# Kernel tuning notes

Measured on AMD Instinct MI355X. Metric: run time of the kernel, lower is better.

The kernel has to match this reference:

```python
import jax, jax.numpy as jnp
from jax import lax
import numpy as np
import math

D_STATE = 2
D_CONV = 4

def _ln(x, g, b, eps=1e-5):
    m = x.mean(-1, keepdims=True)
    v = ((x - m) ** 2).mean(-1, keepdims=True)
    return (x - m) * lax.rsqrt(v + eps) * g + b

def _mamba(x, Win, convw, convb, Wx, Wdt, bdt, Alog, Dp, Wout):
    # x: (b, L, d_model); expand=1 so d_inner == d_model
    b, L, dm = x.shape
    di = Win.shape[0] // 2
    n = Alog.shape[1]
    dtr = Wdt.shape[1]
    k = convw.shape[-1]
    xz = x @ Win.T                                   # (b, L, 2*di)
    xi, z = xz[..., :di], xz[..., di:]
    # causal depthwise conv1d along the sequence axis (pad left k-1, truncate to L)
    xc = jnp.pad(xi, ((0, 0), (k - 1, 0), (0, 0))).transpose(0, 2, 1)  # (b, di, L+k-1)
    xc = lax.conv_general_dilated(xc, convw, (1,), 'VALID',
                                  dimension_numbers=('NCH', 'OIH', 'NCH'),
                                  feature_group_count=di)
    xi = jax.nn.silu(xc.transpose(0, 2, 1) + convb)  # (b, L, di)
    dbl = xi @ Wx.T                                  # (b, L, dtr + 2n)
    dt = jax.nn.softplus(dbl[..., :dtr] @ Wdt.T + bdt)   # (b, L, di)
    Bm = dbl[..., dtr:dtr + n]                       # (b, L, n)
    Cm = dbl[..., dtr + n:]                          # (b, L, n)
    A = -jnp.exp(Alog)                               # (di, n)
    dA = jnp.exp(dt[..., None] * A)                  # (b, L, di, n)
    dBx = dt[..., None] * Bm[:, :, None, :] * xi[..., None]  # (b, L, di, n)

    def step(h, inp):
        dA_t, dBx_t, C_t = inp
        h = dA_t * h + dBx_t                         # (b, di, n)
        return h, jnp.einsum('bdn,bn->bd', h, C_t)

    h0 = jnp.zeros((b, di, n), x.dtype)
    _, ys = lax.scan(step, h0, (dA.transpose(1, 0, 2, 3),
                                dBx.transpose(1, 0, 2, 3),
                                Cm.transpose(1, 0, 2)))
    y = ys.transpose(1, 0, 2) + Dp * xi              # (b, L, di)
    y = y * jax.nn.silu(z)
    return y @ Wout.T                                # (b, L, out_c)

def setup_inputs():
    key = jax.random.key(0)
    ks = jax.random.split(key, 32)
    B, C, H, W = 16, 256, 32, 32
    dm = H * W
    di = dm                      # expand = 1
    dtr = math.ceil(dm / 16)     # dt_rank = 64
    n, k = D_STATE, D_CONV

    def rn(i, shape, s):
        return (jax.random.normal(ks[i], shape) * s).astype(jnp.float32)

    inp = {'x': rn(0, (B, C, H, W), 1.0)}

    def mamba_p(pfx, base):
        inp[pfx + 'Win'] = rn(base, (2 * di, dm), dm ** -0.5)
        inp[pfx + 'convw'] = rn(base + 1, (di, 1, k), k ** -0.5)
        inp[pfx + 'convb'] = jnp.zeros((di,), jnp.float32)
        inp[pfx + 'Wx'] = rn(base + 2, (dtr + 2 * n, di), di ** -0.5)
        inp[pfx + 'Wdt'] = rn(base + 3, (di, dtr), dtr ** -0.5)
        inp[pfx + 'bdt'] = rn(base + 4, (di,), 0.1)
        inp[pfx + 'Alog'] = jnp.log(jnp.broadcast_to(
            jnp.arange(1, n + 1, dtype=jnp.float32), (di, n)))
        inp[pfx + 'D'] = jnp.ones((di,), jnp.float32)
        inp[pfx + 'Wout'] = rn(base + 5, (dm, di), di ** -0.5)  # out_c = sp_dim2^2 = dm

    mamba_p('m1_', 1)
    mamba_p('m2_', 8)
    inp['ln1_g'] = jnp.ones((dm,), jnp.float32)
    inp['ln1_b'] = jnp.zeros((dm,), jnp.float32)
    inp['ln2_g'] = jnp.ones((dm,), jnp.float32)
    inp['ln2_b'] = jnp.zeros((dm,), jnp.float32)
    inp['W_mid'] = rn(15, (C, C), C ** -0.5)   # Linear_Layer inside LIFM_SPA (bias=False)
    inp['W_spa'] = rn(16, (dm, dm), dm ** -0.5)  # linear_spa (nn.Linear default bias)
    inp['b_spa'] = jnp.zeros((dm,), jnp.float32)
    inp['W_res'] = rn(17, (C, C), C ** -0.5)   # lin_chan in residual path (bias=False)
    return inp

def reference(x, m1_Win, m1_convw, m1_convb, m1_Wx, m1_Wdt, m1_bdt, m1_Alog, m1_D, m1_Wout,
              m2_Win, m2_convw, m2_convb, m2_Wx, m2_Wdt, m2_bdt, m2_Alog, m2_D, m2_Wout,
              ln1_g, ln1_b, ln2_g, ln2_b, W_mid, W_spa, b_spa, W_res):
    b, c, h, w = x.shape
    hw = h * w
    # LIFM_SPA path: SSM_spa -> Linear_Layer (channel mix + SiLU) -> SSM_spa
    s = _mamba(x.reshape(b, c, hw), m1_Win, m1_convw, m1_convb,
               m1_Wx, m1_Wdt, m1_bdt, m1_Alog, m1_D, m1_Wout)
    s = _ln(s, ln1_g, ln1_b)                               # (b, c, hw)
    s = jax.nn.silu(jnp.einsum('bcs,oc->bos', s, W_mid))   # channel linear, SiLU (dropout off in eval)
    s = _mamba(s, m2_Win, m2_convw, m2_convb,
               m2_Wx, m2_Wdt, m2_bdt, m2_Alog, m2_D, m2_Wout)
    s = _ln(s, ln2_g, ln2_b)                               # (b, out_c, hw)
    # residual path: spatial linear (+bias) + SiLU, then channel linear + SiLU
    r = jax.nn.silu(x.reshape(b, c, hw) @ W_spa.T + b_spa)
    r = jax.nn.silu(jnp.einsum('bcs,oc->bos', r, W_res))
    return jax.nn.silu(s + r).reshape(b, -1, h, w)
```

## Files before the change

### kernel.cpp

```cpp
#include <hip/hip_runtime.h>
#include <math.h>

#define BATCH 16
#define LSEQ  256
#define DM    1024
#define DI    1024
#define NROWS (BATCH*LSEQ)
#define DTR   64
#define TWO_DI 2048
#define NCH   16
#define CHL   16

typedef __attribute__((ext_vector_type(8))) short short8;
typedef __attribute__((ext_vector_type(4))) float floatx4;
typedef __attribute__((ext_vector_type(4))) unsigned short ushortx4;

__device__ __forceinline__ float siluf(float x) {
    return x / (1.0f + __expf(-x));
}
__device__ __forceinline__ float softplusf(float x) {
    return fmaxf(x, 0.0f) + log1pf(__expf(-fabsf(x)));
}
__device__ __forceinline__ unsigned short f2bf(float f) {
    unsigned int u = __float_as_uint(f);
    u += 0x7fffu + ((u >> 16) & 1u);
    return (unsigned short)(u >> 16);
}
__device__ __forceinline__ float bf2f(unsigned short s) {
    return __uint_as_float(((unsigned int)s) << 16);
}
__device__ __forceinline__ void async16(const short* g, short* l) {
    __builtin_amdgcn_global_load_lds(
        (const __attribute__((address_space(1))) unsigned int*)g,
        (__attribute__((address_space(3))) unsigned int*)l,
        16, 0, 0);
}

__global__ __launch_bounds__(256) void cast8(
    const float* __restrict__ x,    unsigned short* __restrict__ ox,
    const float* __restrict__ w1i,  unsigned short* __restrict__ o1i,
    const float* __restrict__ w1o,  unsigned short* __restrict__ o1o,
    const float* __restrict__ w2i,  unsigned short* __restrict__ o2i,
    const float* __restrict__ w2o,  unsigned short* __restrict__ o2o,
    const float* __restrict__ wsp,  unsigned short* __restrict__ osp,
    const float* __restrict__ wmd,  unsigned short* __restrict__ omd,
    const float* __restrict__ wrs,  unsigned short* __restrict__ ors)
{
    const int b = blockIdx.x;
    const float* in; unsigned short* out; int base;
    if      (b <  4096) { in = x;   out = ox;  base = 0; }
    else if (b <  6144) { in = w1i; out = o1i; base = 4096; }
    else if (b <  7168) { in = w1o; out = o1o; base = 6144; }
    else if (b <  9216) { in = w2i; out = o2i; base = 7168; }
    else if (b < 10240) { in = w2o; out = o2o; base = 9216; }
    else if (b < 11264) { in = wsp; out = osp; base = 10240; }
    else if (b < 11328) { in = wmd; out = omd; base = 11264; }
    else                { in = wrs; out = ors; base = 11328; }
    const size_t i = ((size_t)(b - base) * 256 + threadIdx.x) * 4;
    const float4 v = *(const float4*)(in + i);
    union { unsigned short s[4]; unsigned long long u; } p;
    p.s[0] = f2bf(v.x); p.s[1] = f2bf(v.y);
    p.s[2] = f2bf(v.z); p.s[3] = f2bf(v.w);
    *(unsigned long long*)(out + i) = p.u;
}

template <int EP, int OUT16, int BATW, int FIN>
__global__ __launch_bounds__(64) void gemm1w(
    const short* __restrict__ A,
    const short* __restrict__ W,
    const float* __restrict__ bias,
    const float* __restrict__ Sadd,
    void* __restrict__ Cout,
    int M, int N, int K)
{
    __shared__ short As[2 * 64 * 32];
    __shared__ short Bs[2 * 64 * 32];

    const int bz = BATW ? blockIdx.z : 0;
    const short* Wb = W + (size_t)bz * N * K;
    const size_t cbase = (size_t)bz * M * N;

    const int lane = threadIdx.x;
    const int row0 = blockIdx.y * 64;
    const int col0 = blockIdx.x * 64;

    const int srow  = lane >> 2;
    const int skoff = (lane & 3) * 8;
    const short* gA = A  + (size_t)(row0 + srow) * K + skoff;
    const short* gB = Wb + (size_t)(col0 + srow) * K + skoff;
    short* lA = As + srow * 32 + skoff;
    short* lB = Bs + srow * 32 + skoff;

    const int fr = lane & 15;
    const int fk = (lane >> 4) * 8;

    floatx4 acc[4][4] = {};

    #pragma unroll
    for (int r = 0; r < 4; r++) {
        async16(gA + (size_t)(r * 16) * K, lA + r * 16 * 32);
        async16(gB + (size_t)(r * 16) * K, lB + r * 16 * 32);
    }
    __syncthreads();

    int cur = 0;
    for (int k0 = 0; k0 < K; k0 += 32) {
        const short* Ac = As + cur * 64 * 32;
        const short* Bc = Bs + cur * 64 * 32;
        short8 af[4], bfr[4];
        #pragma unroll
        for (int t = 0; t < 4; t++) {
            af[t]  = *(const short8*)&Ac[(t * 16 + fr) * 32 + fk];
            bfr[t] = *(const short8*)&Bc[(t * 16 + fr) * 32 + fk];
        }
        if (k0 + 32 < K) {
            const int nb = cur ^ 1;
            #pragma unroll
            for (int r = 0; r < 4; r++) {
                async16(gA + (size_t)(r * 16) * K + k0 + 32, lA + (nb * 64 + r * 16) * 32);
                async16(gB + (size_t)(r * 16) * K + k0 + 32, lB + (nb * 64 + r * 16) * 32);
            }
        }
        #pragma unroll
        for (int i = 0; i < 4; i++)
            #pragma unroll
            for (int j = 0; j < 4; j++)
                acc[i][j] = __builtin_amdgcn_mfma_f32_16x16x32_bf16(
                    af[i], bfr[j], acc[i][j], 0, 0, 0);
        __syncthreads();
        cur ^= 1;
    }

    const int crow = row0 + (lane >> 4) * 4;
    const int ccol = col0 + (lane & 15);
    #pragma unroll
    for (int i = 0; i < 4; i++) {
        #pragma unroll
        for (int j = 0; j < 4; j++) {
            const int c = ccol + j * 16;
            #pragma unroll
            for (int r = 0; r < 4; r++) {
                float v = acc[i][j][r];
                if (EP == 1) v = softplusf(v + bias[c]);
                else if (EP == 2) v = siluf(v + bias[c]);
                else if (EP == 3) v = siluf(v);
                const size_t idx = cbase + (size_t)(crow + i * 16 + r) * N + c;
                if (FIN) v = siluf(Sadd[idx] + v);
                if (OUT16) ((unsigned short*)Cout)[idx] = f2bf(v);
                else       ((float*)Cout)[idx] = v;
            }
        }
    }
}

__global__ __launch_bounds__(256) void gemm_nn_wcomb(
    const float* __restrict__ Wdt1, const float* __restrict__ Wx1,
    unsigned short* __restrict__ C1,
    const float* __restrict__ Wdt2, const float* __restrict__ Wx2,
    unsigned short* __restrict__ C2)
{
    const float* Wdt = blockIdx.z ? Wdt2 : Wdt1;
    const float* Wx  = blockIdx.z ? Wx2  : Wx1;
    unsigned short* C16 = blockIdx.z ? C2 : C1;

    __shared__ float Asf[16][64];
    __shared__ float Bsf[16][64];

    const int tid = threadIdx.x;
    const int tx = tid & 15;
    const int ty = tid >> 4;
    const int row0 = blockIdx.y * 64;
    const int col0 = blockIdx.x * 64;
    const int lrow = tid >> 2;
    const int lcol = (tid & 3) * 4;
    const int bk = tid >> 4;
    const int bn = (tid & 15) * 4;

    float acc[4][4] = {};

    for (int k0 = 0; k0 < 64; k0 += 16) {
        const float4 av = *(const float4*)(Wdt + (size_t)(row0 + lrow) * 64 + k0 + lcol);
        Asf[lcol + 0][lrow] = av.x;
        Asf[lcol + 1][lrow] = av.y;
        Asf[lcol + 2][lrow] = av.z;
        Asf[lcol + 3][lrow] = av.w;
        *(float4*)&Bsf[bk][bn] = *(const float4*)(Wx + (size_t)(k0 + bk) * 1024 + col0 + bn);
        __syncthreads();

        #pragma unroll
        for (int kk = 0; kk < 16; kk++) {
            const float4 a = *(const float4*)&Asf[kk][ty * 4];
            const float4 b = *(const float4*)&Bsf[kk][tx * 4];
            const float af[4] = {a.x, a.y, a.z, a.w};
            const float bfv[4] = {b.x, b.y, b.z, b.w};
            #pragma unroll
            for (int i = 0; i < 4; i++)
                #pragma unroll
                for (int j = 0; j < 4; j++)
                    acc[i][j] = fmaf(af[i], bfv[j], acc[i][j]);
        }
        __syncthreads();
    }

    #pragma unroll
    for (int i = 0; i < 4; i++) {
        const int r = row0 + ty * 4 + i;
        #pragma unroll
        for (int j = 0; j < 4; j++)
            C16[(size_t)r * 1024 + col0 + tx * 4 + j] = f2bf(acc[i][j]);
    }
}

__global__ __launch_bounds__(256) void conv_silu_bc(
    const unsigned short* __restrict__ xz16,
    const float* __restrict__ convw,
    const float* __restrict__ convb,
    const float* __restrict__ Wx,
    unsigned short* __restrict__ xi16,
    float* __restrict__ bc)
{
    __shared__ float redc[4][4];
    const int r = blockIdx.x;
    const int l = r & (LSEQ - 1);
    const int tid = threadIdx.x;
    const int d0 = tid * 4;

    ushortx4 x0 = *(const ushortx4*)(xz16 + (size_t)r * TWO_DI + d0);
    ushortx4 x1 = {0,0,0,0}, x2 = {0,0,0,0}, x3 = {0,0,0,0};
    if (l >= 1) x1 = *(const ushortx4*)(xz16 + (size_t)(r - 1) * TWO_DI + d0);
    if (l >= 2) x2 = *(const ushortx4*)(xz16 + (size_t)(r - 2) * TWO_DI + d0);
    if (l >= 3) x3 = *(const ushortx4*)(xz16 + (size_t)(r - 3) * TWO_DI + d0);

    float p0 = 0.f, p1 = 0.f, p2 = 0.f, p3 = 0.f;
    ushortx4 outv;
    #pragma unroll
    for (int j = 0; j < 4; j++) {
        const int d = d0 + j;
        const float4 w = *(const float4*)(convw + d * 4);
        float acc = w.w * bf2f(x0[j]);
        acc = fmaf(w.z, bf2f(x1[j]), acc);
        acc = fmaf(w.y, bf2f(x2[j]), acc);
        acc = fmaf(w.x, bf2f(x3[j]), acc);
        const float v = siluf(acc + convb[d]);
        outv[j] = f2bf(v);
        p0 = fmaf(v, Wx[64 * 1024 + d], p0);
        p1 = fmaf(v, Wx[65 * 1024 + d], p1);
        p2 = fmaf(v, Wx[66 * 1024 + d], p2);
        p3 = fmaf(v, Wx[67 * 1024 + d], p3);
    }
    *(ushortx4*)(xi16 + (size_t)r * DI + d0) = outv;

    #pragma unroll
    for (int o = 32; o; o >>= 1) {
        p0 += __shfl_down(p0, o, 64);
        p1 += __shfl_down(p1, o, 64);
        p2 += __shfl_down(p2, o, 64);
        p3 += __shfl_down(p3, o, 64);
    }
    const int w = tid >> 6, lane = tid & 63;
    if (lane == 0) {
        redc[w][0] = p0; redc[w][1] = p1; redc[w][2] = p2; redc[w][3] = p3;
    }
    __syncthreads();
    if (tid < 4)
        bc[r * 4 + tid] = redc[0][tid] + redc[1][tid] + redc[2][tid] + redc[3][tid];
}

__global__ __launch_bounds__(256) void scan_part1(
    const unsigned short* __restrict__ dt16,
    const unsigned short* __restrict__ xi16,
    const float* __restrict__ bc,
    const float* __restrict__ Alog,
    float4* __restrict__ hc)
{
    const int d  = blockIdx.x * 256 + threadIdx.x;
    const int b  = blockIdx.y;
    const int ch = blockIdx.z;
    const float A0 = -__expf(Alog[d * 2 + 0]);
    const float A1 = -__expf(Alog[d * 2 + 1]);
    float h0 = 0.f, h1 = 0.f, p0 = 1.f, p1 = 1.f;
    const int r0 = b * LSEQ + ch * CHL;
    #pragma unroll 4
    for (int l = 0; l < CHL; l++) {
        const int r = r0 + l;
        const float dtv = bf2f(dt16[(size_t)r * DI + d]);
        const float xiv = bf2f(xi16[(size_t)r * DI + d]);
        const float4 bcv = *(const float4*)(bc + r * 4);
        const float e0 = __expf(dtv * A0);
        const float e1 = __expf(dtv * A1);
        const float dbx = dtv * xiv;
        h0 = fmaf(e0, h0, dbx * bcv.x);
        h1 = fmaf(e1, h1, dbx * bcv.y);
        p0 *= e0; p1 *= e1;
    }
    hc[(size_t)(b * NCH + ch) * DI + d] = make_float4(h0, h1, p0, p1);
}

__global__ __launch_bounds__(256) void scan_carry(
    const float4* __restrict__ hc,
    float2* __restrict__ ci)
{
    const int d = blockIdx.x * 256 + threadIdx.x;
    const int b = blockIdx.y;
    float c0 = 0.f, c1 = 0.f;
    #pragma unroll
    for (int ch = 0; ch < NCH; ch++) {
        const size_t idx = (size_t)(b * NCH + ch) * DI + d;
        const float4 v = hc[idx];
        ci[idx] = make_float2(c0, c1);
        c0 = fmaf(v.z, c0, v.x);
        c1 = fmaf(v.w, c1, v.y);
    }
}

__global__ __launch_bounds__(256) void scan_part2(
    const unsigned short* __restrict__ dt16,
    const unsigned short* __restrict__ xi16,
    const unsigned short* __restrict__ xz16,
    const float* __restrict__ bc,
    const float* __restrict__ Alog,
    const float* __restrict__ Dp,
    const float2* __restrict__ ci,
    unsigned short* __restrict__ yg16)
{
    const int d  = blockIdx.x * 256 + threadIdx.x;
    const int b  = blockIdx.y;
    const int ch = blockIdx.z;
    const float A0 = -__expf(Alog[d * 2 + 0]);
    const float A1 = -__expf(Alog[d * 2 + 1]);
    const float Dv = Dp[d];
    const float2 c = ci[(size_t)(b * NCH + ch) * DI + d];
    float h0 = c.x, h1 = c.y;
    const int r0 = b * LSEQ + ch * CHL;
    #pragma unroll 4
    for (int l = 0; l < CHL; l++) {
        const int r = r0 + l;
        const float dtv = bf2f(dt16[(size_t)r * DI + d]);
        const float xiv = bf2f(xi16[(size_t)r * DI + d]);
        const float4 bcv = *(const float4*)(bc + r * 4);
        const float zv = bf2f(xz16[(size_t)r * TWO_DI + DI + d]);
        const float e0 = __expf(dtv * A0);
        const float e1 = __expf(dtv * A1);
        const float dbx = dtv * xiv;
        h0 = fmaf(e0, h0, dbx * bcv.x);
        h1 = fmaf(e1, h1, dbx * bcv.y);
        const float y = fmaf(h0, bcv.z, fmaf(h1, bcv.w, Dv * xiv));
        yg16[(size_t)r * DI + d] = f2bf(y * siluf(zv));
    }
}

__global__ __launch_bounds__(256) void ln_kernel(
    float* __restrict__ s,
    const float* __restrict__ g,
    const float* __restrict__ bb)
{
    __shared__ float red[8];
    const size_t base = (size_t)blockIdx.x * DM;
    const int t = threadIdx.x;
    float x0 = s[base + t];
    float x1 = s[base + t + 256];
    float x2 = s[base + t + 512];
    float x3 = s[base + t + 768];
    float sum = x0 + x1 + x2 + x3;
    #pragma unroll
    for (int o = 32; o; o >>= 1) sum += __shfl_down(sum, o, 64);
    const int w = t >> 6, lane = t & 63;
    if (lane == 0) red[w] = sum;
    __syncthreads();
    const float m = (red[0] + red[1] + red[2] + red[3]) * (1.0f / 1024.0f);
    const float d0 = x0 - m, d1 = x1 - m, d2 = x2 - m, d3 = x3 - m;
    float ss = d0 * d0 + d1 * d1 + d2 * d2 + d3 * d3;
    #pragma unroll
    for (int o = 32; o; o >>= 1) ss += __shfl_down(ss, o, 64);
    if (lane == 0) red[4 + w] = ss;
    __syncthreads();
    const float var = (red[4] + red[5] + red[6] + red[7]) * (1.0f / 1024.0f);
    const float inv = rsqrtf(var + 1e-5f);
    s[base + t]       = d0 * inv * g[t]       + bb[t];
    s[base + t + 256] = d1 * inv * g[t + 256] + bb[t + 256];
    s[base + t + 512] = d2 * inv * g[t + 512] + bb[t + 512];
    s[base + t + 768] = d3 * inv * g[t + 768] + bb[t + 768];
}

__global__ __launch_bounds__(256) void transpose_cast(
    const float* __restrict__ in, unsigned short* __restrict__ out)
{
    __shared__ float tile[32][33];
    const int b = blockIdx.z;
    const int c0 = blockIdx.y * 32;
    const int s0 = blockIdx.x * 32;
    const int tx = threadIdx.x & 31;
    const int ty = threadIdx.x >> 5;
    const size_t ib = (size_t)b * 256 * 1024;
    const size_t ob = (size_t)b * 1024 * 256;
    #pragma unroll
    for (int i = 0; i < 4; i++)
        tile[tx][ty + i * 8] = in[ib + (size_t)(c0 + ty + i * 8) * 1024 + s0 + tx];
    __syncthreads();
    #pragma unroll
    for (int i = 0; i < 4; i++)
        out[ob + (size_t)(s0 + ty + i * 8) * 256 + c0 + tx] = f2bf(tile[ty + i * 8][tx]);
}

__global__ __launch_bounds__(256) void transpose16(
    const unsigned short* __restrict__ in, unsigned short* __restrict__ out)
{
    __shared__ unsigned short tile[32][34];
    const int b = blockIdx.z;
    const int c0 = blockIdx.y * 32;
    const int s0 = blockIdx.x * 32;
    const int tx = threadIdx.x & 31;
    const int ty = threadIdx.x >> 5;
    const size_t ib = (size_t)b * 256 * 1024;
    const size_t ob = (size_t)b * 1024 * 256;
    #pragma unroll
    for (int i = 0; i < 4; i++)
        tile[tx][ty + i * 8] = in[ib + (size_t)(c0 + ty + i * 8) * 1024 + s0 + tx];
    __syncthreads();
    #pragma unroll
    for (int i = 0; i < 4; i++)
        out[ob + (size_t)(s0 + ty + i * 8) * 256 + c0 + tx] = tile[ty + i * 8][tx];
}

extern "C" void kernel_launch(void* const* d_in, const int* in_sizes, int n_in,
                              void* d_out, int out_size, void* d_ws, size_t ws_size,
                              hipStream_t stream)
{
    const float* x        = (const float*)d_in[0];
    const float* m1_Win   = (const float*)d_in[1];
    const float* m1_convw = (const float*)d_in[2];
    const float* m1_convb = (const float*)d_in[3];
    const float* m1_Wx    = (const float*)d_in[4];
    const float* m1_Wdt   = (const float*)d_in[5];
    const float* m1_bdt   = (const float*)d_in[6];
    const float* m1_Alog  = (const float*)d_in[7];
    const float* m1_D     = (const float*)d_in[8];
    const float* m1_Wout  = (const float*)d_in[9];
    const float* m2_Win   = (const float*)d_in[10];
    const float* m2_convw = (const float*)d_in[11];
    const float* m2_convb = (const float*)d_in[12];
    const float* m2_Wx    = (const float*)d_in[13];
    const float* m2_Wdt   = (const float*)d_in[14];
    const float* m2_bdt   = (const float*)d_in[15];
    const float* m2_Alog  = (const float*)d_in[16];
    const float* m2_D     = (const float*)d_in[17];
    const float* m2_Wout  = (const float*)d_in[18];
    const float* ln1_g    = (const float*)d_in[19];
    const float* ln1_b    = (const float*)d_in[20];
    const float* ln2_g    = (const float*)d_in[21];
    const float* ln2_b    = (const float*)d_in[22];
    const float* W_mid    = (const float*)d_in[23];
    const float* W_spa    = (const float*)d_in[24];
    const float* b_spa    = (const float*)d_in[25];
    const float* W_res    = (const float*)d_in[26];

    float* ws = (float*)d_ws;
    size_t off = 0;
    float* buf_s   = ws + off; off += (size_t)NROWS * DI;
    float* buf_bc  = ws + off; off += (size_t)NROWS * 4;
    float4* buf_hc = (float4*)(ws + off); off += (size_t)BATCH * NCH * DI * 4;
    float2* buf_ci = (float2*)(ws + off); off += (size_t)BATCH * NCH * DI * 2;
    unsigned short* xz16   = (unsigned short*)(ws + off); off += (size_t)NROWS * TWO_DI / 2;
    unsigned short* bx     = (unsigned short*)(ws + off); off += (size_t)NROWS * DI / 2;
    unsigned short* xi16   = (unsigned short*)(ws + off); off += (size_t)NROWS * DI / 2;
    unsigned short* yg16   = (unsigned short*)(ws + off); off += (size_t)NROWS * DI / 2;
    unsigned short* sT16   = (unsigned short*)(ws + off); off += (size_t)NROWS * DI / 2;
    unsigned short* dt16   = (unsigned short*)(ws + off); off += (size_t)NROWS * DI / 2;
    unsigned short* res16  = (unsigned short*)(ws + off); off += (size_t)NROWS * DI / 2;
    unsigned short* win1   = (unsigned short*)(ws + off); off += (size_t)TWO_DI * DM / 2;
    unsigned short* wout1  = (unsigned short*)(ws + off); off += (size_t)DM * DI / 2;
    unsigned short* win2   = (unsigned short*)(ws + off); off += (size_t)TWO_DI * DM / 2;
    unsigned short* wout2  = (unsigned short*)(ws + off); off += (size_t)DM * DI / 2;
    unsigned short* wspa16 = (unsigned short*)(ws + off); off += (size_t)DM * DM / 2;
    unsigned short* wcomb1 = (unsigned short*)(ws + off); off += (size_t)DI * DI / 2;
    unsigned short* wcomb2 = (unsigned short*)(ws + off); off += (size_t)DI * DI / 2;
    unsigned short* wmid16 = (unsigned short*)(ws + off); off += (size_t)LSEQ * LSEQ / 2;
    unsigned short* wres16 = (unsigned short*)(ws + off); off += (size_t)LSEQ * LSEQ / 2;
    unsigned short* t16  = yg16;
    unsigned short* rT16 = sT16;
    (void)ws_size; (void)n_in; (void)in_sizes; (void)out_size;

    const dim3 blk(256);
    const dim3 blk64(64);

    cast8<<<dim3(11392), blk, 0, stream>>>(
        x, bx, m1_Win, win1, m1_Wout, wout1, m2_Win, win2, m2_Wout, wout2,
        W_spa, wspa16, W_mid, wmid16, W_res, wres16);
    gemm_nn_wcomb<<<dim3(16, 16, 2), blk, 0, stream>>>(
        m1_Wdt, m1_Wx, wcomb1, m2_Wdt, m2_Wx, wcomb2);

    auto mamba = [&](const unsigned short* inp16, const unsigned short* win16,
                     const unsigned short* wcomb16, const unsigned short* wout16,
                     const float* convw, const float* convb, const float* Wx,
                     const float* bdt, const float* Alog, const float* Dp,
                     float* out_buf) {
        gemm1w<0, 1, 0, 0><<<dim3(TWO_DI / 64, NROWS / 64), blk64, 0, stream>>>(
            (const short*)inp16, (const short*)win16, nullptr, nullptr,
            (void*)xz16, NROWS, TWO_DI, DM);
        conv_silu_bc<<<dim3(NROWS), blk, 0, stream>>>(
            xz16, convw, convb, Wx, xi16, buf_bc);
        gemm1w<1, 1, 0, 0><<<dim3(DI / 64, NROWS / 64), blk64, 0, stream>>>(
            (const short*)xi16, (const short*)wcomb16, bdt, nullptr,
            (void*)dt16, NROWS, DI, DI);
        scan_part1<<<dim3(DI / 256, BATCH, NCH), blk, 0, stream>>>(
            dt16, xi16, buf_bc, Alog, buf_hc);
        scan_carry<<<dim3(DI / 256, BATCH), blk, 0, stream>>>(buf_hc, buf_ci);
        scan_part2<<<dim3(DI / 256, BATCH, NCH), blk, 0, stream>>>(
            dt16, xi16, xz16, buf_bc, Alog, Dp, buf_ci, yg16);
        gemm1w<0, 0, 0, 0><<<dim3(DM / 64, NROWS / 64), blk64, 0, stream>>>(
            (const short*)yg16, (const short*)wout16, nullptr, nullptr,
            (void*)out_buf, NROWS, DM, DI);
    };

    mamba(bx, win1, wcomb1, wout1, m1_convw, m1_convb, m1_Wx, m1_bdt,
          m1_Alog, m1_D, buf_s);
    ln_kernel<<<dim3(NROWS), blk, 0, stream>>>(buf_s, ln1_g, ln1_b);

    transpose_cast<<<dim3(32, 8, BATCH), blk, 0, stream>>>(buf_s, sT16);
    gemm1w<3, 1, 1, 0><<<dim3(DM / 64, LSEQ / 64, BATCH), blk64, 0, stream>>>(
        (const short*)wmid16, (const short*)sT16, nullptr, nullptr,
        (void*)t16, LSEQ, DM, LSEQ);

    mamba(t16, win2, wcomb2, wout2, m2_convw, m2_convb, m2_Wx, m2_bdt,
          m2_Alog, m2_D, buf_s);
    ln_kernel<<<dim3(NROWS), blk, 0, stream>>>(buf_s, ln2_g, ln2_b);

    gemm1w<2, 1, 0, 0><<<dim3(DM / 64, NROWS / 64), blk64, 0, stream>>>(
        (const short*)bx, (const short*)wspa16, b_spa, nullptr,
        (void*)res16, NROWS, DM, DM);
    transpose16<<<dim3(32, 8, BATCH), blk, 0, stream>>>(res16, rT16);
    gemm1w<3, 0, 1, 1><<<dim3(DM / 64, LSEQ / 64, BATCH), blk64, 0, stream>>>(
        (const short*)wres16, (const short*)rT16, nullptr, buf_s,
        d_out, LSEQ, DM, LSEQ);
}
```

Measured before the change: 472.5 us.

## Split GEMM K dimension across four waves with LDS reduction

```diff
diff --git a/kernel.cpp b/kernel.cpp
--- a/kernel.cpp
+++ b/kernel.cpp
@@ -34,6 +34,9 @@
         (const __attribute__((address_space(1))) unsigned int*)g,
         (__attribute__((address_space(3))) unsigned int*)l,
         16, 0, 0);
+}
+__device__ __forceinline__ void wait_vm0() {
+    __builtin_amdgcn_s_waitcnt(0x0F70);
 }
 
 __global__ __launch_bounds__(256) void cast8(
@@ -65,7 +68,7 @@
 }
 
 template <int EP, int OUT16, int BATW, int FIN>
-__global__ __launch_bounds__(64) void gemm1w(
+__global__ __launch_bounds__(256) void gemm_sk(
     const short* __restrict__ A,
     const short* __restrict__ W,
     const float* __restrict__ bias,
@@ -73,81 +76,98 @@
     void* __restrict__ Cout,
     int M, int N, int K)
 {
-    __shared__ short As[2 * 64 * 32];
-    __shared__ short Bs[2 * 64 * 32];
+    __shared__ float fl[8192];
 
     const int bz = BATW ? blockIdx.z : 0;
     const short* Wb = W + (size_t)bz * N * K;
     const size_t cbase = (size_t)bz * M * N;
 
-    const int lane = threadIdx.x;
+    const int tid  = threadIdx.x;
+    const int w    = tid >> 6;
+    const int lane = tid & 63;
     const int row0 = blockIdx.y * 64;
     const int col0 = blockIdx.x * 64;
 
+    const int Kw  = K >> 2;
+    const int wk0 = w * Kw;
+
     const int srow  = lane >> 2;
     const int skoff = (lane & 3) * 8;
-    const short* gA = A  + (size_t)(row0 + srow) * K + skoff;
-    const short* gB = Wb + (size_t)(col0 + srow) * K + skoff;
-    short* lA = As + srow * 32 + skoff;
-    short* lB = Bs + srow * 32 + skoff;
+    const short* gA = A  + (size_t)(row0 + srow) * K + wk0 + skoff;
+    const short* gB = Wb + (size_t)(col0 + srow) * K + wk0 + skoff;
+    short* st = (short*)fl + w * 4096;
+    short* lA = st + lane * 8;
+    short* lB = lA + 2048;
 
     const int fr = lane & 15;
     const int fk = (lane >> 4) * 8;
+    const int q  = lane >> 4;
 
     floatx4 acc[4][4] = {};
 
-    #pragma unroll
-    for (int r = 0; r < 4; r++) {
-        async16(gA + (size_t)(r * 16) * K, lA + r * 16 * 32);
-        async16(gB + (size_t)(r * 16) * K, lB + r * 16 * 32);
-    }
-    __syncthreads();
-
-    int cur = 0;
-    for (int k0 = 0; k0 < K; k0 += 32) {
-        const short* Ac = As + cur * 64 * 32;
-        const short* Bc = Bs + cur * 64 * 32;
-        short8 af[4], bfr[4];
+    for (int kk = 0; kk < Kw; kk += 32) {
+        #pragma unroll
+        for (int r = 0; r < 4; r++) {
+            async16(gA + (size_t)(r * 16) * K + kk, lA + r * 512);
+            async16(gB + (size_t)(r * 16) * K + kk, lB + r * 512);
+        }
+        wait_vm0();
+        short8 af[4], bf[4];
         #pragma unroll
         for (int t = 0; t < 4; t++) {
-            af[t]  = *(const short8*)&Ac[(t * 16 + fr) * 32 + fk];
-            bfr[t] = *(const short8*)&Bc[(t * 16 + fr) * 32 + fk];
-        }
-        if (k0 + 32 < K) {
-            const int nb = cur ^ 1;
-            #pragma unroll
-            for (int r = 0; r < 4; r++) {
-                async16(gA + (size_t)(r * 16) * K + k0 + 32, lA + (nb * 64 + r * 16) * 32);
-                async16(gB + (size_t)(r * 16) * K + k0 + 32, lB + (nb * 64 + r * 16) * 32);
-            }
+            af[t] = *(const short8*)&st[(t * 16 + fr) * 32 + fk];
+            bf[t] = *(const short8*)&st[2048 + (t * 16 + fr) * 32 + fk];
         }
         #pragma unroll
         for (int i = 0; i < 4; i++)
             #pragma unroll
             for (int j = 0; j < 4; j++)
                 acc[i][j] = __builtin_amdgcn_mfma_f32_16x16x32_bf16(
-                    af[i], bfr[j], acc[i][j], 0, 0, 0);
+                    af[i], bf[j], acc[i][j], 0, 0, 0);
+    }
+
+    #pragma unroll
+    for (int p = 0; p < 2; p++) {
         __syncthreads();
-        cur ^= 1;
-    }
-
-    const int crow = row0 + (lane >> 4) * 4;
-    const int ccol = col0 + (lane & 15);
-    #pragma unroll
-    for (int i = 0; i < 4; i++) {
-        #pragma unroll
-        for (int j = 0; j < 4; j++) {
-            const int c = ccol + j * 16;
+        #pragma unroll
+        for (int i = 0; i < 2; i++) {
             #pragma unroll
-            for (int r = 0; r < 4; r++) {
-                float v = acc[i][j][r];
-                if (EP == 1) v = softplusf(v + bias[c]);
-                else if (EP == 2) v = siluf(v + bias[c]);
-                else if (EP == 3) v = siluf(v);
-                const size_t idx = cbase + (size_t)(crow + i * 16 + r) * N + c;
-                if (FIN) v = siluf(Sadd[idx] + v);
-                if (OUT16) ((unsigned short*)Cout)[idx] = f2bf(v);
-                else       ((float*)Cout)[idx] = v;
+            for (int j = 0; j < 4; j++) {
+                #pragma unroll
+                for (int r = 0; r < 4; r++) {
+                    const int rloc = i * 16 + q * 4 + r;
+                    const int col  = j * 16 + fr;
+                    fl[w * 2048 + rloc * 64 + col] = acc[2 * p + i][j][r];
+                }
+            }
+        }
+        __syncthreads();
+        #pragma unroll
+        for (int v = 0; v < 2; v++) {
+            const int f = tid * 2 + v;
+            const int rloc = f >> 4;
+            const int cb = (f & 15) * 4;
+            const float* p0 = &fl[rloc * 64 + cb];
+            const float4 s0 = *(const float4*)(p0);
+            const float4 s1 = *(const float4*)(p0 + 2048);
+            const float4 s2 = *(const float4*)(p0 + 4096);
+            const float4 s3 = *(const float4*)(p0 + 6144);
+            float sv[4] = { s0.x + s1.x + s2.x + s3.x,
+                            s0.y + s1.y + s2.y + s3.y,
+                            s0.z + s1.z + s2.z + s3.z,
+                            s0.w + s1.w + s2.w + s3.w };
+            const int grow = row0 + p * 32 + rloc;
+            #pragma unroll
+            for (int e = 0; e < 4; e++) {
+                const int c = col0 + cb + e;
+                float vv = sv[e];
+                if (EP == 1) vv = softplusf(vv + bias[c]);
+                else if (EP == 2) vv = siluf(vv + bias[c]);
+                else if (EP == 3) vv = siluf(vv);
+                const size_t idx = cbase + (size_t)grow * N + c;
+                if (FIN) vv = siluf(Sadd[idx] + vv);
+                if (OUT16) ((unsigned short*)Cout)[idx] = f2bf(vv);
+                else       ((float*)Cout)[idx] = vv;
             }
         }
     }
@@ -481,7 +501,6 @@
     (void)ws_size; (void)n_in; (void)in_sizes; (void)out_size;
 
     const dim3 blk(256);
-    const dim3 blk64(64);
 
     cast8<<<dim3(11392), blk, 0, stream>>>(
         x, bx, m1_Win, win1, m1_Wout, wout1, m2_Win, win2, m2_Wout, wout2,
@@ -494,12 +513,12 @@
                      const float* convw, const float* convb, const float* Wx,
                      const float* bdt, const float* Alog, const float* Dp,
                      float* out_buf) {
-        gemm1w<0, 1, 0, 0><<<dim3(TWO_DI / 64, NROWS / 64), blk64, 0, stream>>>(
+        gemm_sk<0, 1, 0, 0><<<dim3(TWO_DI / 64, NROWS / 64), blk, 0, stream>>>(
             (const short*)inp16, (const short*)win16, nullptr, nullptr,
             (void*)xz16, NROWS, TWO_DI, DM);
         conv_silu_bc<<<dim3(NROWS), blk, 0, stream>>>(
             xz16, convw, convb, Wx, xi16, buf_bc);
-        gemm1w<1, 1, 0, 0><<<dim3(DI / 64, NROWS / 64), blk64, 0, stream>>>(
+        gemm_sk<1, 1, 0, 0><<<dim3(DI / 64, NROWS / 64), blk, 0, stream>>>(
             (const short*)xi16, (const short*)wcomb16, bdt, nullptr,
             (void*)dt16, NROWS, DI, DI);
         scan_part1<<<dim3(DI / 256, BATCH, NCH), blk, 0, stream>>>(
@@ -507,7 +526,7 @@
         scan_carry<<<dim3(DI / 256, BATCH), blk, 0, stream>>>(buf_hc, buf_ci);
         scan_part2<<<dim3(DI / 256, BATCH, NCH), blk, 0, stream>>>(
             dt16, xi16, xz16, buf_bc, Alog, Dp, buf_ci, yg16);
-        gemm1w<0, 0, 0, 0><<<dim3(DM / 64, NROWS / 64), blk64, 0, stream>>>(
+        gemm_sk<0, 0, 0, 0><<<dim3(DM / 64, NROWS / 64), blk, 0, stream>>>(
             (const short*)yg16, (const short*)wout16, nullptr, nullptr,
             (void*)out_buf, NROWS, DM, DI);
     };
@@ -517,7 +536,7 @@
     ln_kernel<<<dim3(NROWS), blk, 0, stream>>>(buf_s, ln1_g, ln1_b);
 
     transpose_cast<<<dim3(32, 8, BATCH), blk, 0, stream>>>(buf_s, sT16);
-    gemm1w<3, 1, 1, 0><<<dim3(DM / 64, LSEQ / 64, BATCH), blk64, 0, stream>>>(
+    gemm_sk<3, 1, 1, 0><<<dim3(DM / 64, LSEQ / 64, BATCH), blk, 0, stream>>>(
         (const short*)wmid16, (const short*)sT16, nullptr, nullptr,
         (void*)t16, LSEQ, DM, LSEQ);
 
@@ -525,11 +544,11 @@
           m2_Alog, m2_D, buf_s);
     ln_kernel<<<dim3(NROWS), blk, 0, stream>>>(buf_s, ln2_g, ln2_b);
 
-    gemm1w<2, 1, 0, 0><<<dim3(DM / 64, NROWS / 64), blk64, 0, stream>>>(
+    gemm_sk<2, 1, 0, 0><<<dim3(DM / 64, NROWS / 64), blk, 0, stream>>>(
         (const short*)bx, (const short*)wspa16, b_spa, nullptr,
         (void*)res16, NROWS, DM, DM);
     transpose16<<<dim3(32, 8, BATCH), blk, 0, stream>>>(res16, rT16);
-    gemm1w<3, 0, 1, 1><<<dim3(DM / 64, LSEQ / 64, BATCH), blk64, 0, stream>>>(
+    gemm_sk<3, 0, 1, 1><<<dim3(DM / 64, LSEQ / 64, BATCH), blk, 0, stream>>>(
         (const short*)wres16, (const short*)rT16, nullptr, buf_s,
         d_out, LSEQ, DM, LSEQ);
 }
```

After: 463.4 us. About the same (-1.9%).
